# Kernel tuning notes

Measured on AMD Instinct MI355X. Metric: run time of the kernel, lower is better.

The kernel has to match this reference:

```python
import jax, jax.numpy as jnp
import numpy as np
import math

SQRT7 = math.sqrt(7.0)
EPS = 1e-05


def int4_quant(x):
    # absmean scaling to [-8, 7]; out = x_q * (beta*sqrt7) / sqrt7
    beta = jnp.mean(jnp.abs(x), axis=-1, keepdims=True)
    x_q = jnp.clip(jnp.round(x * SQRT7 / (beta + EPS)), -8, 7)
    return x_q * (beta * SQRT7) / SQRT7


def int8_quant(x):
    # absmax scaling to [-128, 127]
    gamma = jnp.max(jnp.abs(x), axis=-1, keepdims=True)
    x_q = jnp.clip(jnp.round(x * 127.0 / (gamma + EPS)), -128, 127)
    return x_q * gamma / 127.0


def bitlinear(x, w, scale):
    # ternary (1.58-bit) weight fake-quant: round(W / mean|W|) clamped to {-1,0,1}
    w_mean = jnp.mean(jnp.abs(w))
    w_q = jnp.clip(jnp.round(w / (w_mean + EPS)), -1.0, 1.0)
    w_eff = w_q * w_mean * scale  # [out, in]
    return jnp.einsum('...i,oi->...o', x, w_eff)


def setup_inputs() -> dict:
    key = jax.random.key(0)
    ks = jax.random.split(key, 4)
    H, I = 4096, 11008
    B, S = 2, 2048
    # kaiming_uniform(a=sqrt(5)) -> bound = 1/sqrt(fan_in)
    x = jax.random.normal(ks[0], (B, S, H), dtype=jnp.float32)
    w_gate = jax.random.uniform(ks[1], (I, H), jnp.float32, -1.0, 1.0) / np.sqrt(H)
    w_up = jax.random.uniform(ks[2], (I, H), jnp.float32, -1.0, 1.0) / np.sqrt(H)
    w_down = jax.random.uniform(ks[3], (H, I), jnp.float32, -1.0, 1.0) / np.sqrt(I)
    ones = jnp.ones((1,), jnp.float32)
    return {"x": x, "w_gate": w_gate, "w_up": w_up, "w_down": w_down,
            "s_gate": ones, "s_up": ones, "s_down": ones}


def reference(x, w_gate, w_up, w_down, s_gate, s_up, s_down):
    xq = int4_quant(x)                          # [B,S,H]
    gate = bitlinear(xq, w_gate, s_gate)        # [B,S,I]
    up = bitlinear(xq, w_up, s_up)              # [B,S,I]
    gate = jnp.square(jax.nn.relu(gate))        # ReLU^2 gate
    inter = int8_quant(up * gate)               # [B,S,I]
    return bitlinear(inter, w_down, s_down)     # [B,S,H]
```

## Files before the change

### kernel.cpp

```cpp
#include <hip/hip_runtime.h>
#include <stdint.h>


typedef int i32x4 __attribute__((ext_vector_type(4)));
typedef short s16x8 __attribute__((ext_vector_type(8)));

#define HD 4096
#define ID 11008
#define MD 4096
#define WN 45088768
#define N1 22016
#define QEPS 1e-5f
#define SQRT7 2.6457513110645907f

__device__ __forceinline__ void mfma_a(i32x4& acc, i32x4 a, i32x4 b) {
  asm volatile("v_mfma_i32_16x16x64_i8 %0, %1, %2, %0"
               : "+a"(acc) : "v"(a), "v"(b));
}

__device__ __forceinline__ void gload_lds16(const char* g, char* l) {
  __builtin_amdgcn_global_load_lds((const __attribute__((address_space(1))) void*)g,
                                   (__attribute__((address_space(3))) void*)l, 16, 0, 0);
}

__device__ __forceinline__ void stage64q(const char* __restrict__ g, int ldk,
                                         char* lds, int t256) {
  int r = t256 >> 2, sl = (t256 & 3) ^ ((t256 >> 3) & 3);
  const char* gp = g + (size_t)r * ldk + (sl << 4);
  char* lp = lds + t256 * 16;
#pragma unroll
  for (int i = 0; i < 4; ++i) {
    gload_lds16(gp, lp);
    gp += (size_t)64 * ldk;
    lp += 4096;
  }
}

__device__ __forceinline__ void gemm_core(const char* __restrict__ ga,
                                          const char* __restrict__ gb,
                                          int ldk, int nt, char* lds,
                                          i32x4 (&acc)[8][8], int w, int l) {
  const int t256 = w * 64 + l;
  const int wr = (w >> 1) * 128, wc = (w & 1) * 128;
  const int lr = l & 15;
  const int sw4 = (((l >> 4) ^ ((l >> 1) & 3)) << 4);
#pragma unroll
  for (int pt = 0; pt < 3; ++pt) {
    stage64q(ga + (size_t)pt * 64, ldk, lds + pt * 32768, t256);
    stage64q(gb + (size_t)pt * 64, ldk, lds + pt * 32768 + 16384, t256);
  }
  for (int t = 0; t < nt; ++t) {
    if (t + 2 < nt)      asm volatile("s_waitcnt vmcnt(16)" ::: "memory");
    else if (t + 1 < nt) asm volatile("s_waitcnt vmcnt(8)" ::: "memory");
    else                 asm volatile("s_waitcnt vmcnt(0)" ::: "memory");
    __builtin_amdgcn_s_barrier();
    const char* Ab = lds + (t & 3) * 32768;
    const char* Bb = Ab + 16384;
    char* pre = lds + ((t + 3) & 3) * 32768;
    if (t + 3 < nt) stage64q(ga + (size_t)(t + 3) * 64, ldk, pre, t256);
    i32x4 af[8], bf[8];
#pragma unroll
    for (int i = 0; i < 8; ++i)
      af[i] = *(const i32x4*)(Ab + (wr + i * 16 + lr) * 64 + sw4);
#pragma unroll
    for (int i = 0; i < 4; ++i)
      bf[i] = *(const i32x4*)(Bb + (wc + i * 16 + lr) * 64 + sw4);
#pragma unroll
    for (int n = 0; n < 4; ++n)
#pragma unroll
      for (int m = 0; m < 8; ++m)
        mfma_a(acc[m][n], af[m], bf[n]);
    if (t + 3 < nt) stage64q(gb + (size_t)(t + 3) * 64, ldk, pre + 16384, t256);
#pragma unroll
    for (int i = 4; i < 8; ++i)
      bf[i] = *(const i32x4*)(Bb + (wc + i * 16 + lr) * 64 + sw4);
#pragma unroll
    for (int n = 4; n < 8; ++n)
#pragma unroll
      for (int m = 0; m < 8; ++m)
        mfma_a(acc[m][n], af[m], bf[n]);
  }
}

__global__ __launch_bounds__(256, 1) void gemm1_kernel(
    const char* __restrict__ A, const char* __restrict__ B, short* __restrict__ C) {
  __shared__ __align__(16) char lds[131072];
  int t = threadIdx.x, w = t >> 6, l = t & 63;
  int wgid = ((int)blockIdx.x & 7) * 172 + ((int)blockIdx.x >> 3);
  int bm = wgid & 15, bn = wgid >> 4;
  i32x4 acc[8][8] = {};
  gemm_core(A + (size_t)bm * 256 * HD, B + (size_t)bn * 256 * HD, HD, HD / 64,
            lds, acc, w, l);
  int wr = (w >> 1) * 128, wc = (w & 1) * 128, lr = l & 15, lj = (l >> 4) * 4;
#pragma unroll
  for (int mi = 0; mi < 8; ++mi) {
    int row = bm * 256 + wr + mi * 16 + lj;
#pragma unroll
    for (int ni = 0; ni < 8; ++ni) {
      int col = bn * 256 + wc + ni * 16 + lr;
#pragma unroll
      for (int j = 0; j < 4; ++j) {
        int v = acc[mi][ni][j];
        v = v < -32768 ? -32768 : (v > 32767 ? 32767 : v);
        C[(size_t)(row + j) * N1 + col] = (short)v;
      }
    }
  }
}

__global__ __launch_bounds__(256, 1) void gemm_down_kernel(
    const char* __restrict__ A, const char* __restrict__ B, float* __restrict__ out,
    const float* __restrict__ gammaF, const double* __restrict__ sums,
    const float* __restrict__ sd) {
  __shared__ __align__(16) char lds[131072];
  int t = threadIdx.x, w = t >> 6, l = t & 63;
  int wgid = ((int)blockIdx.x & 7) * 32 + ((int)blockIdx.x >> 3);
  int bm = wgid & 15, bn = wgid >> 4;
  i32x4 acc[8][8] = {};
  gemm_core(A + (size_t)bm * 256 * ID, B + (size_t)bn * 256 * ID, ID, ID / 64,
            lds, acc, w, l);
  float wdm = (float)(sums[2] * (1.0 / (double)WN)) * sd[0] * (1.f / 127.f);
  int wr = (w >> 1) * 128, wc = (w & 1) * 128, lr = l & 15, lj = (l >> 4) * 4;
#pragma unroll
  for (int mi = 0; mi < 8; ++mi) {
    int row = bm * 256 + wr + mi * 16 + lj;
    float sa[4];
#pragma unroll
    for (int j = 0; j < 4; ++j) sa[j] = gammaF[row + j] * wdm;
#pragma unroll
    for (int ni = 0; ni < 8; ++ni) {
      int col = bn * 256 + wc + ni * 16 + lr;
#pragma unroll
      for (int j = 0; j < 4; ++j)
        out[(size_t)(row + j) * HD + col] = (float)acc[mi][ni][j] * sa[j];
    }
  }
}

__device__ __forceinline__ int pack4div(float4 v, float mul, float den, float lo, float hi) {
  int a = (int)fminf(fmaxf(rintf((v.x * mul) / den), lo), hi);
  int b = (int)fminf(fmaxf(rintf((v.y * mul) / den), lo), hi);
  int c = (int)fminf(fmaxf(rintf((v.z * mul) / den), lo), hi);
  int d = (int)fminf(fmaxf(rintf((v.w * mul) / den), lo), hi);
  return (a & 255) | ((b & 255) << 8) | ((c & 255) << 16) | ((d & 255) << 24);
}

__global__ __launch_bounds__(256) void abssum_kernel(const float4* __restrict__ w,
                                                     int n8, double* __restrict__ out) {
  float s = 0.f;
  int stride = gridDim.x * blockDim.x;
  for (int i = blockIdx.x * blockDim.x + threadIdx.x; i < n8; i += stride) {
    float4 v0 = w[i * 2], v1 = w[i * 2 + 1];
    s += fabsf(v0.x) + fabsf(v0.y) + fabsf(v0.z) + fabsf(v0.w);
    s += fabsf(v1.x) + fabsf(v1.y) + fabsf(v1.z) + fabsf(v1.w);
  }
#pragma unroll
  for (int off = 32; off > 0; off >>= 1) s += __shfl_down(s, off);
  __shared__ float red[4];
  int l = threadIdx.x & 63, wv = threadIdx.x >> 6;
  if (l == 0) red[wv] = s;
  __syncthreads();
  if (threadIdx.x == 0) {
    double tt = (double)red[0] + (double)red[1] + (double)red[2] + (double)red[3];
    atomicAdd(out, tt);
  }
}

__global__ __launch_bounds__(256) void quantx_kernel(const float* __restrict__ x,
                                                     char* __restrict__ xq,
                                                     float* __restrict__ scale_x) {
  int row = blockIdx.x;
  const float4* xr = (const float4*)(x + (size_t)row * HD);
  int t = threadIdx.x;
  float4 v[4];
  float s = 0.f;
#pragma unroll
  for (int k = 0; k < 4; ++k) {
    v[k] = xr[t + k * 256];
    s += fabsf(v[k].x) + fabsf(v[k].y) + fabsf(v[k].z) + fabsf(v[k].w);
  }
#pragma unroll
  for (int off = 32; off > 0; off >>= 1) s += __shfl_down(s, off);
  __shared__ float red[4];
  int l = t & 63, wv = t >> 6;
  if (l == 0) red[wv] = s;
  __syncthreads();
  float beta = (red[0] + red[1] + red[2] + red[3]) * (1.f / (float)HD);
  if (t == 0) scale_x[row] = (beta * SQRT7) / SQRT7;
  float den = beta + QEPS;
  int* qr = (int*)(xq + (size_t)row * HD);
#pragma unroll
  for (int k = 0; k < 4; ++k)
    qr[t + k * 256] = pack4div(v[k], SQRT7, den, -8.f, 7.f);
}

__global__ __launch_bounds__(256) void quantw_kernel(const float4* __restrict__ w,
                                                     int4* __restrict__ wq,
                                                     const double* __restrict__ sum) {
  float mean = (float)(*sum * (1.0 / (double)WN));
  float den = mean + QEPS;
  int n16 = WN / 16;
  int stride = gridDim.x * blockDim.x;
  for (int i = blockIdx.x * blockDim.x + threadIdx.x; i < n16; i += stride) {
    float4 v0 = w[i * 4 + 0], v1 = w[i * 4 + 1], v2 = w[i * 4 + 2], v3 = w[i * 4 + 3];
    int4 o;
    o.x = pack4div(v0, 1.f, den, -1.f, 1.f);
    o.y = pack4div(v1, 1.f, den, -1.f, 1.f);
    o.z = pack4div(v2, 1.f, den, -1.f, 1.f);
    o.w = pack4div(v3, 1.f, den, -1.f, 1.f);
    wq[i] = o;
  }
}

__global__ __launch_bounds__(256) void combine_kernel(
    const short* __restrict__ C, const float* __restrict__ scale_x,
    const double* __restrict__ sums, const float* __restrict__ sg,
    const float* __restrict__ su, float* __restrict__ gammaF,
    char* __restrict__ hq) {
  int row = blockIdx.x, t = threadIdx.x;
  float gm = (float)(sums[0] * (1.0 / (double)WN)) * sg[0];
  float um = (float)(sums[1] * (1.0 / (double)WN)) * su[0];
  float sx = scale_x[row];
  float sxg = sx * gm, sxu = sx * um;
  const s16x8* g8 = (const s16x8*)(C + (size_t)row * N1);
  const s16x8* u8 = (const s16x8*)(C + (size_t)row * N1 + ID);
  float hv[6][8];
  float m = 0.f;
#pragma unroll
  for (int k = 0; k < 6; ++k) {
    int c = t + k * 256;
    if (c < ID / 8) {
      s16x8 gi = __builtin_nontemporal_load(&g8[c]);
      s16x8 ui = __builtin_nontemporal_load(&u8[c]);
#pragma unroll
      for (int e = 0; e < 8; ++e) {
        float rg = fmaxf((float)gi[e] * sxg, 0.f);
        hv[k][e] = ((float)ui[e] * sxu) * (rg * rg);
        m = fmaxf(m, fabsf(hv[k][e]));
      }
    }
  }
#pragma unroll
  for (int off = 32; off > 0; off >>= 1) m = fmaxf(m, __shfl_xor(m, off));
  __shared__ float red[4];
  if ((t & 63) == 0) red[t >> 6] = m;
  __syncthreads();
  float gamma = fmaxf(fmaxf(red[0], red[1]), fmaxf(red[2], red[3]));
  if (t == 0) gammaF[row] = gamma;
  float den = gamma + QEPS;
  int2* hr = (int2*)(hq + (size_t)row * ID);
#pragma unroll
  for (int k = 0; k < 6; ++k) {
    int c = t + k * 256;
    if (c < ID / 8) {
      int2 o;
      o.x = pack4div(make_float4(hv[k][0], hv[k][1], hv[k][2], hv[k][3]), 127.f, den, -128.f, 127.f);
      o.y = pack4div(make_float4(hv[k][4], hv[k][5], hv[k][6], hv[k][7]), 127.f, den, -128.f, 127.f);
      hr[c] = o;
    }
  }
}

extern "C" void kernel_launch(void* const* d_in, const int* in_sizes, int n_in,
                              void* d_out, int out_size, void* d_ws, size_t ws_size,
                              hipStream_t stream) {
  (void)in_sizes; (void)n_in; (void)out_size; (void)ws_size;
  const float* x = (const float*)d_in[0];
  const float* w_gate = (const float*)d_in[1];
  const float* w_up = (const float*)d_in[2];
  const float* w_down = (const float*)d_in[3];
  const float* s_gate = (const float*)d_in[4];
  const float* s_up = (const float*)d_in[5];
  const float* s_down = (const float*)d_in[6];
  float* out = (float*)d_out;

  char* p = (char*)d_ws;
  double* sums = (double*)p;
  float* gammaF = (float*)(p + 256);
  float* scale_x = (float*)(p + 256 + 16384);
  char* xq = p + 33024;
  char* wgq = xq + 16777216UL;
  char* wuq = wgq + (size_t)WN;
  char* wdq = wuq + (size_t)WN;
  short* C16 = (short*)(wdq + (size_t)WN);
  char* hq = (char*)C16 + 180355072UL;

  (void)hipMemsetAsync(p, 0, 256, stream);

  abssum_kernel<<<2048, 256, 0, stream>>>((const float4*)w_down, WN / 8, sums + 2);
  quantw_kernel<<<2048, 256, 0, stream>>>((const float4*)w_down, (int4*)wdq, sums + 2);
  abssum_kernel<<<2048, 256, 0, stream>>>((const float4*)w_gate, WN / 8, sums + 0);
  quantw_kernel<<<2048, 256, 0, stream>>>((const float4*)w_gate, (int4*)wgq, sums + 0);
  abssum_kernel<<<2048, 256, 0, stream>>>((const float4*)w_up, WN / 8, sums + 1);
  quantw_kernel<<<2048, 256, 0, stream>>>((const float4*)w_up, (int4*)wuq, sums + 1);

  quantx_kernel<<<MD, 256, 0, stream>>>(x, xq, scale_x);

  gemm1_kernel<<<1376, 256, 0, stream>>>(xq, wgq, C16);

  combine_kernel<<<MD, 256, 0, stream>>>(C16, scale_x, sums, s_gate, s_up, gammaF, hq);

  gemm_down_kernel<<<256, 256, 0, stream>>>(hq, wdq, out, gammaF, sums, s_down);
}
```

Baseline: 830.6 us.

## Switch int8 GEMM core from 16x16x64 to 32x32x32 MFMA tiles

Replaces the 16x16x64 int8 MFMA instruction with the 32x32x32 variant in the shared GEMM core. The LDS fragment loads are rearranged into 32-row blocks with two K-half slots, and both epilogues are remapped to the 32x32 accumulator layout. Larger MFMA tiles mean fewer LDS fragment reads and fewer instructions per unit of work. The cost is a more complex output mapping and a different LDS bank access pattern, which may cause conflicts.

```diff
diff --git a/kernel.cpp b/kernel.cpp
--- a/kernel.cpp
+++ b/kernel.cpp
@@ -3,6 +3,7 @@
 
 
 typedef int i32x4 __attribute__((ext_vector_type(4)));
+typedef int i32x16 __attribute__((ext_vector_type(16)));
 typedef short s16x8 __attribute__((ext_vector_type(8)));
 
 #define HD 4096
@@ -13,8 +14,8 @@
 #define QEPS 1e-5f
 #define SQRT7 2.6457513110645907f
 
-__device__ __forceinline__ void mfma_a(i32x4& acc, i32x4 a, i32x4 b) {
-  asm volatile("v_mfma_i32_16x16x64_i8 %0, %1, %2, %0"
+__device__ __forceinline__ void mfma32(i32x16& acc, i32x4 a, i32x4 b) {
+  asm volatile("v_mfma_i32_32x32x32_i8 %0, %1, %2, %0"
                : "+a"(acc) : "v"(a), "v"(b));
 }
 
@@ -39,11 +40,12 @@
 __device__ __forceinline__ void gemm_core(const char* __restrict__ ga,
                                           const char* __restrict__ gb,
                                           int ldk, int nt, char* lds,
-                                          i32x4 (&acc)[8][8], int w, int l) {
+                                          i32x16 (&acc)[4][4], int w, int l) {
   const int t256 = w * 64 + l;
   const int wr = (w >> 1) * 128, wc = (w & 1) * 128;
-  const int lr = l & 15;
-  const int sw4 = (((l >> 4) ^ ((l >> 1) & 3)) << 4);
+  const int l31 = l & 31, kh = l >> 5, sx = (l >> 1) & 3;
+  const int slot0 = ((0 + kh) ^ sx) << 4;
+  const int slot1 = ((2 + kh) ^ sx) << 4;
 #pragma unroll
   for (int pt = 0; pt < 3; ++pt) {
     stage64q(ga + (size_t)pt * 64, ldk, lds + pt * 32768, t256);
@@ -58,27 +60,40 @@
     const char* Bb = Ab + 16384;
     char* pre = lds + ((t + 3) & 3) * 32768;
     if (t + 3 < nt) stage64q(ga + (size_t)(t + 3) * 64, ldk, pre, t256);
-    i32x4 af[8], bf[8];
-#pragma unroll
-    for (int i = 0; i < 8; ++i)
-      af[i] = *(const i32x4*)(Ab + (wr + i * 16 + lr) * 64 + sw4);
-#pragma unroll
-    for (int i = 0; i < 4; ++i)
-      bf[i] = *(const i32x4*)(Bb + (wc + i * 16 + lr) * 64 + sw4);
-#pragma unroll
-    for (int n = 0; n < 4; ++n)
-#pragma unroll
-      for (int m = 0; m < 8; ++m)
-        mfma_a(acc[m][n], af[m], bf[n]);
+    i32x4 af[4][2], bf[4][2];
+#pragma unroll
+    for (int rb = 0; rb < 4; ++rb) {
+      const char* rp = Ab + (wr + rb * 32 + l31) * 64;
+      af[rb][0] = *(const i32x4*)(rp + slot0);
+      af[rb][1] = *(const i32x4*)(rp + slot1);
+    }
+#pragma unroll
+    for (int nb = 0; nb < 2; ++nb) {
+      const char* rp = Bb + (wc + nb * 32 + l31) * 64;
+      bf[nb][0] = *(const i32x4*)(rp + slot0);
+      bf[nb][1] = *(const i32x4*)(rp + slot1);
+    }
+#pragma unroll
+    for (int nb = 0; nb < 2; ++nb)
+#pragma unroll
+      for (int rb = 0; rb < 4; ++rb) {
+        mfma32(acc[rb][nb], af[rb][0], bf[nb][0]);
+        mfma32(acc[rb][nb], af[rb][1], bf[nb][1]);
+      }
     if (t + 3 < nt) stage64q(gb + (size_t)(t + 3) * 64, ldk, pre + 16384, t256);
 #pragma unroll
-    for (int i = 4; i < 8; ++i)
-      bf[i] = *(const i32x4*)(Bb + (wc + i * 16 + lr) * 64 + sw4);
-#pragma unroll
-    for (int n = 4; n < 8; ++n)
-#pragma unroll
-      for (int m = 0; m < 8; ++m)
-        mfma_a(acc[m][n], af[m], bf[n]);
+    for (int nb = 2; nb < 4; ++nb) {
+      const char* rp = Bb + (wc + nb * 32 + l31) * 64;
+      bf[nb][0] = *(const i32x4*)(rp + slot0);
+      bf[nb][1] = *(const i32x4*)(rp + slot1);
+    }
+#pragma unroll
+    for (int nb = 2; nb < 4; ++nb)
+#pragma unroll
+      for (int rb = 0; rb < 4; ++rb) {
+        mfma32(acc[rb][nb], af[rb][0], bf[nb][0]);
+        mfma32(acc[rb][nb], af[rb][1], bf[nb][1]);
+      }
   }
 }
 
@@ -88,21 +103,24 @@
   int t = threadIdx.x, w = t >> 6, l = t & 63;
   int wgid = ((int)blockIdx.x & 7) * 172 + ((int)blockIdx.x >> 3);
   int bm = wgid & 15, bn = wgid >> 4;
-  i32x4 acc[8][8] = {};
+  i32x16 acc[4][4] = {};
   gemm_core(A + (size_t)bm * 256 * HD, B + (size_t)bn * 256 * HD, HD, HD / 64,
             lds, acc, w, l);
-  int wr = (w >> 1) * 128, wc = (w & 1) * 128, lr = l & 15, lj = (l >> 4) * 4;
-#pragma unroll
-  for (int mi = 0; mi < 8; ++mi) {
-    int row = bm * 256 + wr + mi * 16 + lj;
-#pragma unroll
-    for (int ni = 0; ni < 8; ++ni) {
-      int col = bn * 256 + wc + ni * 16 + lr;
-#pragma unroll
-      for (int j = 0; j < 4; ++j) {
-        int v = acc[mi][ni][j];
-        v = v < -32768 ? -32768 : (v > 32767 ? 32767 : v);
-        C[(size_t)(row + j) * N1 + col] = (short)v;
+  int wr = (w >> 1) * 128, wc = (w & 1) * 128, l31 = l & 31, h4 = (l >> 5) * 4;
+#pragma unroll
+  for (int mi = 0; mi < 4; ++mi) {
+#pragma unroll
+    for (int q = 0; q < 4; ++q) {
+      int rbase = bm * 256 + wr + mi * 32 + 8 * q + h4;
+#pragma unroll
+      for (int ni = 0; ni < 4; ++ni) {
+        int col = bn * 256 + wc + ni * 32 + l31;
+#pragma unroll
+        for (int j = 0; j < 4; ++j) {
+          int v = acc[mi][ni][q * 4 + j];
+          v = v < -32768 ? -32768 : (v > 32767 ? 32767 : v);
+          C[(size_t)(rbase + j) * N1 + col] = (short)v;
+        }
       }
     }
   }
@@ -116,23 +134,25 @@
   int t = threadIdx.x, w = t >> 6, l = t & 63;
   int wgid = ((int)blockIdx.x & 7) * 32 + ((int)blockIdx.x >> 3);
   int bm = wgid & 15, bn = wgid >> 4;
-  i32x4 acc[8][8] = {};
+  i32x16 acc[4][4] = {};
   gemm_core(A + (size_t)bm * 256 * ID, B + (size_t)bn * 256 * ID, ID, ID / 64,
             lds, acc, w, l);
   float wdm = (float)(sums[2] * (1.0 / (double)WN)) * sd[0] * (1.f / 127.f);
-  int wr = (w >> 1) * 128, wc = (w & 1) * 128, lr = l & 15, lj = (l >> 4) * 4;
-#pragma unroll
-  for (int mi = 0; mi < 8; ++mi) {
-    int row = bm * 256 + wr + mi * 16 + lj;
-    float sa[4];
-#pragma unroll
-    for (int j = 0; j < 4; ++j) sa[j] = gammaF[row + j] * wdm;
-#pragma unroll
-    for (int ni = 0; ni < 8; ++ni) {
-      int col = bn * 256 + wc + ni * 16 + lr;
-#pragma unroll
-      for (int j = 0; j < 4; ++j)
-        out[(size_t)(row + j) * HD + col] = (float)acc[mi][ni][j] * sa[j];
+  int wr = (w >> 1) * 128, wc = (w & 1) * 128, l31 = l & 31, h4 = (l >> 5) * 4;
+#pragma unroll
+  for (int mi = 0; mi < 4; ++mi) {
+#pragma unroll
+    for (int q = 0; q < 4; ++q) {
+      int rbase = bm * 256 + wr + mi * 32 + 8 * q + h4;
+      float4 g4 = *(const float4*)&gammaF[rbase];
+      float sa[4] = {g4.x * wdm, g4.y * wdm, g4.z * wdm, g4.w * wdm};
+#pragma unroll
+      for (int ni = 0; ni < 4; ++ni) {
+        int col = bn * 256 + wc + ni * 32 + l31;
+#pragma unroll
+        for (int j = 0; j < 4; ++j)
+          out[(size_t)(rbase + j) * HD + col] = (float)acc[mi][ni][q * 4 + j] * sa[j];
+      }
     }
   }
 }
```

New measurement: 862.0 us. 1.04x slower.
